# Kernel optimization log

Hardware: AMD Instinct MI355X
Metric: run time of the kernel (lower is better)

The kernel has to match this reference:

```python
import jax, jax.numpy as jnp
import numpy as np

B, H, W, C = 16, 64, 64, 512
NH, WS, SS, P = 16, 8, 4, 4
HID = 2048
N = WS * WS
HD = C // NH
SCALE = HD ** -0.5
NWIN = (H // WS) * (W // WS)

# static azimuth angle table (N, N): (w_i - w_j) * 2*pi / W_res  (W_res = input_resolution[1])
_wf = np.arange(N) % WS
AZ_ANG = (_wf[:, None] - _wf[None, :]).astype(np.float32) * np.float32(2.0 * np.pi / W)


def _shift_mask():
    # standard SW-MSA region mask: 0 within same region, -100 across regions
    img = np.zeros((H, W), dtype=np.float32)
    cnt = 0
    for hs in (slice(0, -WS), slice(-WS, -SS), slice(-SS, None)):
        for ws_ in (slice(0, -WS), slice(-WS, -SS), slice(-SS, None)):
            img[hs, ws_] = cnt
            cnt += 1
    win = img.reshape(H // WS, WS, W // WS, WS).transpose(0, 2, 1, 3).reshape(-1, N)
    diff = win[:, None, :] - win[:, :, None]
    return np.where(diff != 0, -100.0, 0.0).astype(np.float32)

MASK = _shift_mask()  # (NWIN, N, N)


def _ln(x, g, b):
    m = x.mean(-1, keepdims=True)
    v = ((x - m) ** 2).mean(-1, keepdims=True)
    return (x - m) / jnp.sqrt(v + 1e-5) * g + b


def _forward(x, D, gamma1, beta1, Wqkv, bqkv, Wproj, bproj, a_p, b_p, a_r, b_r, gamma2, beta2, W1, b1, W2, b2):
    shortcut = x
    h = _ln(x, gamma1, beta1).reshape(B, H, W, C)
    d = D.reshape(B, H, W)
    # cyclic shift
    h = jnp.roll(h, (-SS, -SS), axis=(1, 2))
    d = jnp.roll(d, (-SS, -SS), axis=(1, 2))
    # window partition -> (B*NWIN, N, C) and depth windows (B*NWIN, N)
    hw = h.reshape(B, H // WS, WS, W // WS, WS, C).transpose(0, 1, 3, 2, 4, 5).reshape(-1, N, C)
    dw = d.reshape(B, H // WS, WS, W // WS, WS).transpose(0, 1, 3, 2, 4).reshape(-1, N)
    Bw = B * NWIN
    qkv = (hw @ Wqkv + bqkv).reshape(Bw, N, 3, NH, HD)
    q, k, v = qkv[:, :, 0], qkv[:, :, 1], qkv[:, :, 2]
    attn = jnp.einsum('bnhd,bmhd->bhnm', q * SCALE, k)
    # Fourier azimuth bias A_phi: (NH, N, N), input-independent within forward
    i_arr = jnp.arange(1, P + 1, dtype=x.dtype)
    az_i = i_arr[:, None, None] * jnp.asarray(AZ_ANG, dtype=x.dtype)  # (P, N, N)
    A_phi = (jnp.einsum('pnm,ph->hnm', jnp.cos(az_i), a_p[1:])
             + jnp.einsum('pnm,ph->hnm', jnp.sin(az_i), b_p)) / P + a_p[0][:, None, None]
    # Fourier radial bias A_r from input-dependent depth differences; r_max hardcoded to 2 in source
    radD = dw[:, None, :] - dw[:, :, None]  # (Bw, N, N): D_j - D_i
    ang = radD[None] * (np.pi * i_arr)[:, None, None, None]  # (P, Bw, N, N); 2*pi*i/r_max = pi*i
    A_r = (jnp.einsum('pbnm,ph->bhnm', jnp.cos(ang), a_r[1:])
           + jnp.einsum('pbnm,ph->bhnm', jnp.sin(ang), b_r)) / P + a_r[0][None, :, None, None]
    attn = attn + A_phi[None] + A_r
    attn = attn.reshape(B, NWIN, NH, N, N) + jnp.asarray(MASK, dtype=x.dtype)[None, :, None]
    attn = jax.nn.softmax(attn.reshape(Bw, NH, N, N), axis=-1)
    out = jnp.einsum('bhnm,bmhd->bnhd', attn, v).reshape(Bw, N, C)
    out = out @ Wproj + bproj
    # window reverse + reverse shift
    out = out.reshape(B, H // WS, W // WS, WS, WS, C).transpose(0, 1, 3, 2, 4, 5).reshape(B, H, W, C)
    out = jnp.roll(out, (SS, SS), axis=(1, 2)).reshape(B, H * W, C)
    x2 = shortcut + out
    h2 = _ln(x2, gamma2, beta2)
    h2 = jax.nn.gelu(h2 @ W1 + b1, approximate=False) @ W2 + b2
    return x2 + h2


def setup_inputs() -> dict:
    key = jax.random.key(0)
    ks = jax.random.split(key, 10)
    s = 0.02
    return {
        'x': jax.random.normal(ks[0], (B, H * W, C), jnp.float32),
        'D': jax.random.uniform(ks[1], (B, H * W), jnp.float32),
        'gamma1': jnp.ones((C,), jnp.float32),
        'beta1': jnp.zeros((C,), jnp.float32),
        'Wqkv': jax.random.normal(ks[2], (C, 3 * C), jnp.float32) * s,
        'bqkv': jnp.zeros((3 * C,), jnp.float32),
        'Wproj': jax.random.normal(ks[3], (C, C), jnp.float32) * s,
        'bproj': jnp.zeros((C,), jnp.float32),
        'a_p': jax.random.normal(ks[4], (P + 1, NH), jnp.float32) * s,
        'b_p': jax.random.normal(ks[5], (P, NH), jnp.float32) * s,
        'a_r': jax.random.normal(ks[6], (P + 1, NH), jnp.float32) * s,
        'b_r': jax.random.normal(ks[7], (P, NH), jnp.float32) * s,
        'gamma2': jnp.ones((C,), jnp.float32),
        'beta2': jnp.zeros((C,), jnp.float32),
        'W1': jax.random.normal(ks[8], (C, HID), jnp.float32) * s,
        'b1': jnp.zeros((HID,), jnp.float32),
        'W2': jax.random.normal(ks[9], (HID, C), jnp.float32) * s,
        'b2': jnp.zeros((C,), jnp.float32),
    }


def reference(x, D, gamma1, beta1, Wqkv, bqkv, Wproj, bproj, a_p, b_p, a_r, b_r, gamma2, beta2, W1, b1, W2, b2):
    return _forward(x, D, gamma1, beta1, Wqkv, bqkv, Wproj, bproj, a_p, b_p, a_r, b_r, gamma2, beta2, W1, b1, W2, b2)
```

## Files before the change

kernel.cpp:

```cpp
#include <hip/hip_runtime.h>
#include <hip/hip_bf16.h>
#include <cstdint>


typedef __attribute__((ext_vector_type(8))) short short8;
typedef __attribute__((ext_vector_type(4))) float f32x4;
typedef unsigned short u16;

__device__ __forceinline__ u16 f2bf(float f) {
  __hip_bfloat16 h = __float2bfloat16(f);
  return *reinterpret_cast<u16*>(&h);
}

__device__ __forceinline__ void gld_lds16(const u16* g, u16* l) {
  __builtin_amdgcn_global_load_lds(
      (const __attribute__((address_space(1))) void*)g,
      (__attribute__((address_space(3))) void*)l, 16, 0, 0);
}

__global__ void wt_convert(const float* __restrict__ W, u16* __restrict__ Wt,
                           int K, int N) {
  __shared__ float tile[32][33];
  const int n0 = blockIdx.x * 32, k0 = blockIdx.y * 32;
  const int tx = threadIdx.x & 31, ty = threadIdx.x >> 5;
#pragma unroll
  for (int r = ty; r < 32; r += 8)
    tile[r][tx] = W[(size_t)(k0 + r) * N + n0 + tx];
  __syncthreads();
#pragma unroll
  for (int r = ty; r < 32; r += 8)
    Wt[(size_t)(n0 + r) * K + k0 + tx] = f2bf(tile[tx][r]);
}

__global__ void aphi_kernel(const float* __restrict__ a_p,
                            const float* __restrict__ b_p,
                            float* __restrict__ aphi) {
  const int idx = blockIdx.x * 256 + threadIdx.x;
  const int h = idx >> 12, n = (idx >> 6) & 63, m = idx & 63;
  const float ang = (float)((n & 7) - (m & 7)) * 0.09817477042468103f;
  float v = a_p[h];
#pragma unroll
  for (int p = 0; p < 4; ++p) {
    float s, c;
    __sincosf((float)(p + 1) * ang, &s, &c);
    v += (c * a_p[(p + 1) * 16 + h] + s * b_p[p * 16 + h]) * 0.25f;
  }
  aphi[idx] = v;
}

__global__ __launch_bounds__(64) void ln1_win(
    const float* __restrict__ x, const float* __restrict__ D,
    const float* __restrict__ gamma, const float* __restrict__ beta,
    u16* __restrict__ xw, float* __restrict__ dwout) {
  const int r = blockIdx.x;
  const int lane = threadIdx.x;
  const int w = r >> 6, n = r & 63;
  const int bb = w >> 6, nw = w & 63;
  const int wh = nw >> 3, ww = nw & 7;
  const int i = n >> 3, j = n & 7;
  const int sh = (wh * 8 + i + 4) & 63;
  const int sw = (ww * 8 + j + 4) & 63;
  const size_t src = ((size_t)bb * 4096 + sh * 64 + sw) * 512;
  float4 v0 = *(const float4*)(x + src + lane * 8);
  float4 v1 = *(const float4*)(x + src + lane * 8 + 4);
  float vv[8] = {v0.x, v0.y, v0.z, v0.w, v1.x, v1.y, v1.z, v1.w};
  float s = 0.f, s2 = 0.f;
#pragma unroll
  for (int e = 0; e < 8; ++e) { s += vv[e]; s2 += vv[e] * vv[e]; }
#pragma unroll
  for (int off = 32; off > 0; off >>= 1) {
    s += __shfl_xor(s, off);
    s2 += __shfl_xor(s2, off);
  }
  const float mean = s * (1.0f / 512.0f);
  const float var = s2 * (1.0f / 512.0f) - mean * mean;
  const float rstd = rsqrtf(var + 1e-5f);
  const int c0 = lane * 8;
  u16 ob[8];
#pragma unroll
  for (int e = 0; e < 8; ++e)
    ob[e] = f2bf((vv[e] - mean) * rstd * gamma[c0 + e] + beta[c0 + e]);
  *(short8*)(xw + (size_t)r * 512 + c0) = *(short8*)ob;
  if (lane == 0) dwout[r] = D[(size_t)bb * 4096 + sh * 64 + sw];
}

__global__ __launch_bounds__(64) void ln2_kernel(
    const float* __restrict__ xin, const float* __restrict__ gamma,
    const float* __restrict__ beta, u16* __restrict__ h2) {
  const int r = blockIdx.x;
  const int lane = threadIdx.x;
  const size_t src = (size_t)r * 512;
  float4 v0 = *(const float4*)(xin + src + lane * 8);
  float4 v1 = *(const float4*)(xin + src + lane * 8 + 4);
  float vv[8] = {v0.x, v0.y, v0.z, v0.w, v1.x, v1.y, v1.z, v1.w};
  float s = 0.f, s2 = 0.f;
#pragma unroll
  for (int e = 0; e < 8; ++e) { s += vv[e]; s2 += vv[e] * vv[e]; }
#pragma unroll
  for (int off = 32; off > 0; off >>= 1) {
    s += __shfl_xor(s, off);
    s2 += __shfl_xor(s2, off);
  }
  const float mean = s * (1.0f / 512.0f);
  const float var = s2 * (1.0f / 512.0f) - mean * mean;
  const float rstd = rsqrtf(var + 1e-5f);
  const int c0 = lane * 8;
  u16 ob[8];
#pragma unroll
  for (int e = 0; e < 8; ++e)
    ob[e] = f2bf((vv[e] - mean) * rstd * gamma[c0 + e] + beta[c0 + e]);
  *(short8*)(h2 + src + c0) = *(short8*)ob;
}

template <int EPI, int GX>
__global__ __launch_bounds__(512, 4) void gemm_bt(
    const u16* __restrict__ A, const u16* __restrict__ Bt,
    const float* __restrict__ bias, u16* __restrict__ outb,
    float* __restrict__ outf, const float* __restrict__ addsrc,
    int M, int N, int K) {
  __shared__ __align__(16) u16 sA[256 * 32];
  __shared__ __align__(16) u16 sB[128 * 32];
  const int t = threadIdx.x;
  const int lid = blockIdx.x;
  const int xcd = lid & 7;
  const int tt = lid >> 3;
  const int bx = tt % GX;
  const int by = (tt / GX) * 8 + xcd;
  const int m0 = by * 256, n0 = bx * 128;
  const int lane = t & 63, wave = t >> 6;
  const int wm = wave >> 1, wn = wave & 1;
  const int l15 = lane & 15, quad = lane >> 4;

  f32x4 acc[4][4];
#pragma unroll
  for (int i = 0; i < 4; ++i)
#pragma unroll
    for (int j = 0; j < 4; ++j) acc[i][j] = (f32x4){0.f, 0.f, 0.f, 0.f};

  const int sa0 = t, sa1 = t + 512, sb0 = t;
  const int ra0 = sa0 >> 2, pa0 = sa0 & 3, la0 = pa0 ^ ((ra0 >> 1) & 3);
  const int ra1 = sa1 >> 2, pa1 = sa1 & 3, la1 = pa1 ^ ((ra1 >> 1) & 3);
  const int rb0 = sb0 >> 2, pb0 = sb0 & 3, lb0c = pb0 ^ ((rb0 >> 1) & 3);
  const u16* Ag0 = A + (size_t)(m0 + ra0) * K + la0 * 8;
  const u16* Ag1 = A + (size_t)(m0 + ra1) * K + la1 * 8;
  const u16* Bg0 = Bt + (size_t)(n0 + rb0) * K + lb0c * 8;
  u16* lA0 = &sA[sa0 * 8];
  u16* lA1 = &sA[sa1 * 8];
  u16* lB0 = &sB[sb0 * 8];

  for (int kk = 0; kk < K; kk += 32) {
    gld_lds16(Ag0 + kk, lA0);
    gld_lds16(Ag1 + kk, lA1);
    gld_lds16(Bg0 + kk, lB0);
    __syncthreads();
    short8 af[4], bf[4];
#pragma unroll
    for (int i = 0; i < 4; ++i) {
      const int ra = wm * 64 + i * 16 + l15;
      const int ca = quad ^ ((ra >> 1) & 3);
      af[i] = *(const short8*)&sA[ra * 32 + ca * 8];
      const int rb = wn * 64 + i * 16 + l15;
      const int cb = quad ^ ((rb >> 1) & 3);
      bf[i] = *(const short8*)&sB[rb * 32 + cb * 8];
    }
#pragma unroll
    for (int i = 0; i < 4; ++i)
#pragma unroll
      for (int j = 0; j < 4; ++j)
        acc[i][j] = __builtin_amdgcn_mfma_f32_16x16x32_bf16(af[i], bf[j],
                                                            acc[i][j], 0, 0, 0);
    __syncthreads();
  }

#pragma unroll
  for (int i = 0; i < 4; ++i) {
    const int gr0 = m0 + wm * 64 + i * 16 + quad * 4;
#pragma unroll
    for (int j = 0; j < 4; ++j) {
      const int gc = n0 + wn * 64 + j * 16 + l15;
      const float bv = bias[gc];
      f32x4 a = acc[i][j];
#pragma unroll
      for (int r = 0; r < 4; ++r) {
        const int gr = gr0 + r;
        float val = a[r] + bv;
        if (EPI == 0) {
          outb[(size_t)gr * N + gc] = f2bf(val);
        } else if (EPI == 1) {
          val = 0.5f * val * (1.0f + erff(val * 0.7071067811865475f));
          outb[(size_t)gr * N + gc] = f2bf(val);
        } else if (EPI == 2) {
          const int w = gr >> 6, n = gr & 63;
          const int bb = w >> 6, nw = w & 63;
          const int wh = nw >> 3, ww = nw & 7;
          const int ii = n >> 3, jj = n & 7;
          const int th = (wh * 8 + ii + 4) & 63;
          const int tw = (ww * 8 + jj + 4) & 63;
          const size_t tok = (size_t)bb * 4096 + th * 64 + tw;
          outf[tok * 512 + gc] = addsrc[tok * 512 + gc] + val;
        } else {
          outf[(size_t)gr * N + gc] += val;
        }
      }
    }
  }
}

__device__ __forceinline__ int bandf(int p) {
  return p < 56 ? 0 : (p < 60 ? 1 : 2);
}

__global__ void attn_kernel(const u16* __restrict__ qkv,
                            const float* __restrict__ dw,
                            const float* __restrict__ aphi,
                            const float* __restrict__ a_r,
                            const float* __restrict__ b_r,
                            u16* __restrict__ outp) {
  __shared__ __align__(16) u16 sVt[32 * 72];
  __shared__ __align__(16) u16 sP[64 * 72];
  __shared__ float sdw[64];
  const int bid = blockIdx.x;
  const int w = bid >> 4, h = bid & 15;
  const int lane = threadIdx.x;
  const int l15 = lane & 15, quad = lane >> 4;
  const int nw = w & 63, wh = nw >> 3, wwc = nw & 7;

  const float ar0 = a_r[h];
  float arc[4], brc[4];
#pragma unroll
  for (int p = 0; p < 4; ++p) {
    arc[p] = a_r[(p + 1) * 16 + h] * 0.25f;
    brc[p] = b_r[p * 16 + h] * 0.25f;
  }

  sdw[lane] = dw[w * 64 + lane];
  {
    const u16* vrow = qkv + (size_t)(w * 64 + lane) * 1536 + 1024 + h * 32;
    u16 vt[32];
#pragma unroll
    for (int c = 0; c < 4; ++c)
      *(short8*)&vt[c * 8] = *(const short8*)(vrow + c * 8);
#pragma unroll
    for (int d = 0; d < 32; ++d) sVt[d * 72 + lane] = vt[d];
  }
  __syncthreads();

  short8 qf[4], kf[4];
#pragma unroll
  for (int tq = 0; tq < 4; ++tq) {
    qf[tq] = *(const short8*)(qkv + (size_t)(w * 64 + tq * 16 + l15) * 1536 +
                              h * 32 + quad * 8);
    kf[tq] = *(const short8*)(qkv + (size_t)(w * 64 + tq * 16 + l15) * 1536 +
                              512 + h * 32 + quad * 8);
  }

  float dn[16];
  int rq[16];
#pragma unroll
  for (int tm = 0; tm < 4; ++tm)
#pragma unroll
    for (int r = 0; r < 4; ++r) {
      const int n = tm * 16 + quad * 4 + r;
      dn[tm * 4 + r] = sdw[n];
      rq[tm * 4 + r] = bandf(wh * 8 + (n >> 3)) * 4 + bandf(wwc * 8 + (n & 7));
    }
  float dmv[4];
  int rk[4];
#pragma unroll
  for (int tn = 0; tn < 4; ++tn) {
    const int m = tn * 16 + l15;
    dmv[tn] = sdw[m];
    rk[tn] = bandf(wh * 8 + (m >> 3)) * 4 + bandf(wwc * 8 + (m & 7));
  }

  f32x4 S[4][4];
  const float SCALE = 0.17677669529663687f;
#pragma unroll
  for (int tm = 0; tm < 4; ++tm)
#pragma unroll
    for (int tn = 0; tn < 4; ++tn) {
      f32x4 s = __builtin_amdgcn_mfma_f32_16x16x32_bf16(
          qf[tm], kf[tn], (f32x4){0.f, 0.f, 0.f, 0.f}, 0, 0, 0);
      const int m = tn * 16 + l15;
#pragma unroll
      for (int r = 0; r < 4; ++r) {
        const int n = tm * 16 + quad * 4 + r;
        const float rad = dmv[tn] - dn[tm * 4 + r];
        float s1, c1;
        __sincosf(3.14159265358979323846f * rad, &s1, &c1);
        const float c2 = c1 * c1 - s1 * s1, t2 = 2.f * s1 * c1;
        const float c3 = c2 * c1 - t2 * s1, t3 = t2 * c1 + c2 * s1;
        const float c4 = c2 * c2 - t2 * t2, t4 = 2.f * t2 * c2;
        const float arv = ar0 + c1 * arc[0] + s1 * brc[0] + c2 * arc[1] +
                          t2 * brc[1] + c3 * arc[2] + t3 * brc[2] +
                          c4 * arc[3] + t4 * brc[3];
        float val = s[r] * SCALE + aphi[h * 4096 + n * 64 + m] + arv;
        if (rq[tm * 4 + r] != rk[tn]) val -= 100.f;
        S[tm][tn][r] = val;
      }
    }

#pragma unroll
  for (int tm = 0; tm < 4; ++tm)
#pragma unroll
    for (int r = 0; r < 4; ++r) {
      float mx = fmaxf(fmaxf(S[tm][0][r], S[tm][1][r]),
                       fmaxf(S[tm][2][r], S[tm][3][r]));
#pragma unroll
      for (int off = 1; off < 16; off <<= 1) mx = fmaxf(mx, __shfl_xor(mx, off));
      float sm = 0.f;
#pragma unroll
      for (int tn = 0; tn < 4; ++tn) {
        const float e = __expf(S[tm][tn][r] - mx);
        S[tm][tn][r] = e;
        sm += e;
      }
#pragma unroll
      for (int off = 1; off < 16; off <<= 1) sm += __shfl_xor(sm, off);
      const float inv = 1.0f / sm;
      const int n = tm * 16 + quad * 4 + r;
#pragma unroll
      for (int tn = 0; tn < 4; ++tn)
        sP[n * 72 + tn * 16 + l15] = f2bf(S[tm][tn][r] * inv);
    }
  __syncthreads();

  short8 vf[2][2];
#pragma unroll
  for (int ks = 0; ks < 2; ++ks)
#pragma unroll
    for (int td = 0; td < 2; ++td)
      vf[ks][td] =
          *(const short8*)&sVt[(td * 16 + l15) * 72 + ks * 32 + quad * 8];
  f32x4 O[4][2];
#pragma unroll
  for (int tm = 0; tm < 4; ++tm)
#pragma unroll
    for (int td = 0; td < 2; ++td) O[tm][td] = (f32x4){0.f, 0.f, 0.f, 0.f};
#pragma unroll
  for (int tm = 0; tm < 4; ++tm)
#pragma unroll
    for (int ks = 0; ks < 2; ++ks) {
      const short8 pf =
          *(const short8*)&sP[(tm * 16 + l15) * 72 + ks * 32 + quad * 8];
#pragma unroll
      for (int td = 0; td < 2; ++td)
        O[tm][td] =
            __builtin_amdgcn_mfma_f32_16x16x32_bf16(pf, vf[ks][td], O[tm][td], 0, 0, 0);
    }

#pragma unroll
  for (int tm = 0; tm < 4; ++tm)
#pragma unroll
    for (int td = 0; td < 2; ++td)
#pragma unroll
      for (int r = 0; r < 4; ++r) {
        const int n = tm * 16 + quad * 4 + r;
        const int d = td * 16 + l15;
        outp[(size_t)(w * 64 + n) * 512 + h * 32 + d] = f2bf(O[tm][td][r]);
      }
}

extern "C" void kernel_launch(void* const* d_in, const int* in_sizes, int n_in,
                              void* d_out, int out_size, void* d_ws,
                              size_t ws_size, hipStream_t stream) {
  const float* x = (const float*)d_in[0];
  const float* D = (const float*)d_in[1];
  const float* gamma1 = (const float*)d_in[2];
  const float* beta1 = (const float*)d_in[3];
  const float* Wqkv = (const float*)d_in[4];
  const float* bqkv = (const float*)d_in[5];
  const float* Wproj = (const float*)d_in[6];
  const float* bproj = (const float*)d_in[7];
  const float* a_p = (const float*)d_in[8];
  const float* b_p = (const float*)d_in[9];
  const float* a_r = (const float*)d_in[10];
  const float* b_r = (const float*)d_in[11];
  const float* gamma2 = (const float*)d_in[12];
  const float* beta2 = (const float*)d_in[13];
  const float* W1 = (const float*)d_in[14];
  const float* b1 = (const float*)d_in[15];
  const float* W2 = (const float*)d_in[16];
  const float* b2 = (const float*)d_in[17];
  float* out = (float*)d_out;

  char* ws = (char*)d_ws;
  const size_t OFF_XW = 0;
  const size_t OFF_QKV = 67108864;
  const size_t OFF_AO = 335544320;
  const size_t OFF_WQT = 402653184;
  const size_t OFF_WPT = 404226048;
  const size_t OFF_W1T = 404750336;
  const size_t OFF_W2T = 406847488;
  const size_t OFF_APHI = 408944640;
  const size_t OFF_DW = 409206784;
  const size_t TOTAL = 409468928;
  if (ws_size < TOTAL) return;

  u16* xw = (u16*)(ws + OFF_XW);
  u16* qkv = (u16*)(ws + OFF_QKV);
  u16* ao = (u16*)(ws + OFF_AO);
  u16* WqkvT = (u16*)(ws + OFF_WQT);
  u16* WprojT = (u16*)(ws + OFF_WPT);
  u16* W1T = (u16*)(ws + OFF_W1T);
  u16* W2T = (u16*)(ws + OFF_W2T);
  float* aphiW = (float*)(ws + OFF_APHI);
  float* dwW = (float*)(ws + OFF_DW);
  u16* h2 = xw;
  u16* gbuf = qkv;

  wt_convert<<<dim3(48, 16), 256, 0, stream>>>(Wqkv, WqkvT, 512, 1536);
  wt_convert<<<dim3(16, 16), 256, 0, stream>>>(Wproj, WprojT, 512, 512);
  wt_convert<<<dim3(64, 16), 256, 0, stream>>>(W1, W1T, 512, 2048);
  wt_convert<<<dim3(16, 64), 256, 0, stream>>>(W2, W2T, 2048, 512);
  aphi_kernel<<<256, 256, 0, stream>>>(a_p, b_p, aphiW);
  ln1_win<<<65536, 64, 0, stream>>>(x, D, gamma1, beta1, xw, dwW);

  gemm_bt<0, 12><<<12 * 256, 512, 0, stream>>>(xw, WqkvT, bqkv, qkv, nullptr,
                                               nullptr, 65536, 1536, 512);
  attn_kernel<<<16384, 64, 0, stream>>>(qkv, dwW, aphiW, a_r, b_r, ao);
  gemm_bt<2, 4><<<4 * 256, 512, 0, stream>>>(ao, WprojT, bproj, nullptr, out,
                                             x, 65536, 512, 512);
  ln2_kernel<<<65536, 64, 0, stream>>>(out, gamma2, beta2, h2);
  gemm_bt<1, 16><<<16 * 256, 512, 0, stream>>>(h2, W1T, b1, gbuf, nullptr,
                                               nullptr, 65536, 2048, 512);
  gemm_bt<3, 4><<<4 * 256, 512, 0, stream>>>(gbuf, W2T, b2, nullptr, out,
                                             nullptr, 65536, 512, 2048);
}
```

Baseline: 1.097 ms.

## Triple-buffer GEMM LDS tiles with async global-to-LDS prefetch

The bf16 GEMM kernel now keeps three LDS stages for the A and B tiles and prefetches two k-tiles ahead using direct global-to-LDS loads. Hand-written vmcnt waits and barriers replace the per-iteration syncthreads, so global load latency can overlap with MFMA work. The cost is three times the LDS footprint, 72KB per block, which can limit occupancy below the launch_bounds target of 4 blocks. It also depends on vmcnt counting that is fragile if the compiler inserts other vector memory ops.

```diff
diff --git a/kernel.cpp b/kernel.cpp
--- a/kernel.cpp
+++ b/kernel.cpp
@@ -118,8 +118,8 @@
     const float* __restrict__ bias, u16* __restrict__ outb,
     float* __restrict__ outf, const float* __restrict__ addsrc,
     int M, int N, int K) {
-  __shared__ __align__(16) u16 sA[256 * 32];
-  __shared__ __align__(16) u16 sB[128 * 32];
+  __shared__ __align__(16) u16 sA[3][256 * 32];
+  __shared__ __align__(16) u16 sB[3][128 * 32];
   const int t = threadIdx.x;
   const int lid = blockIdx.x;
   const int xcd = lid & 7;
@@ -144,32 +144,51 @@
   const u16* Ag0 = A + (size_t)(m0 + ra0) * K + la0 * 8;
   const u16* Ag1 = A + (size_t)(m0 + ra1) * K + la1 * 8;
   const u16* Bg0 = Bt + (size_t)(n0 + rb0) * K + lb0c * 8;
-  u16* lA0 = &sA[sa0 * 8];
-  u16* lA1 = &sA[sa1 * 8];
-  u16* lB0 = &sB[sb0 * 8];
-
-  for (int kk = 0; kk < K; kk += 32) {
-    gld_lds16(Ag0 + kk, lA0);
-    gld_lds16(Ag1 + kk, lA1);
-    gld_lds16(Bg0 + kk, lB0);
-    __syncthreads();
-    short8 af[4], bf[4];
+
+  const int NT = K >> 5;
+
+#pragma unroll
+  for (int pt = 0; pt < 3; ++pt) {
+    gld_lds16(Ag0 + pt * 32, &sA[pt][sa0 * 8]);
+    gld_lds16(Ag1 + pt * 32, &sA[pt][sa1 * 8]);
+    gld_lds16(Bg0 + pt * 32, &sB[pt][sb0 * 8]);
+  }
+
+  int buf = 0;
+  for (int kt = 0; kt < NT; ++kt) {
+    if (kt + 2 < NT) {
+      asm volatile("s_waitcnt vmcnt(6)\n\ts_barrier" ::: "memory");
+    } else if (kt + 1 < NT) {
+      asm volatile("s_waitcnt vmcnt(3)\n\ts_barrier" ::: "memory");
+    } else {
+      asm volatile("s_waitcnt vmcnt(0)\n\ts_barrier" ::: "memory");
+    }
+    const u16* bufA = sA[buf];
+    const u16* bufB = sB[buf];
+    short8 af[4], bfr[4];
 #pragma unroll
     for (int i = 0; i < 4; ++i) {
       const int ra = wm * 64 + i * 16 + l15;
       const int ca = quad ^ ((ra >> 1) & 3);
-      af[i] = *(const short8*)&sA[ra * 32 + ca * 8];
+      af[i] = *(const short8*)&bufA[ra * 32 + ca * 8];
       const int rb = wn * 64 + i * 16 + l15;
       const int cb = quad ^ ((rb >> 1) & 3);
-      bf[i] = *(const short8*)&sB[rb * 32 + cb * 8];
+      bfr[i] = *(const short8*)&bufB[rb * 32 + cb * 8];
     }
 #pragma unroll
     for (int i = 0; i < 4; ++i)
 #pragma unroll
       for (int j = 0; j < 4; ++j)
-        acc[i][j] = __builtin_amdgcn_mfma_f32_16x16x32_bf16(af[i], bf[j],
+        acc[i][j] = __builtin_amdgcn_mfma_f32_16x16x32_bf16(af[i], bfr[j],
                                                             acc[i][j], 0, 0, 0);
-    __syncthreads();
+    asm volatile("s_waitcnt lgkmcnt(0)\n\ts_barrier" ::: "memory");
+    if (kt + 3 < NT) {
+      const int kk = (kt + 3) * 32;
+      gld_lds16(Ag0 + kk, &sA[buf][sa0 * 8]);
+      gld_lds16(Ag1 + kk, &sA[buf][sa1 * 8]);
+      gld_lds16(Bg0 + kk, &sB[buf][sb0 * 8]);
+    }
+    buf = (buf == 2) ? 0 : buf + 1;
   }
 
 #pragma unroll
```

Result: faster. 1.075 ms (-2.0%).

## Rewrite GEMM as double-buffered 256x256 tile pipeline with interleaved prefetch

Applied to the files above, without the earlier changes.

Replaces the single-buffered 256x128 GEMM mainloop with a 256x256 tile and a 64-wide K step. LDS is double-buffered and split into two K-halves, and the next tile's A and B loads are issued between MFMA phases under explicit vmcnt waits, barriers and s_setprio. The aim is to hide global-to-LDS latency and raise MFMA work per LDS byte. In exchange it uses 128KB of LDS and 128 accumulator registers per thread, so occupancy drops to about one block per CU. Grid sizes are halved to match the wider N tile.

```diff
diff --git a/kernel.cpp b/kernel.cpp
--- a/kernel.cpp
+++ b/kernel.cpp
@@ -112,69 +112,152 @@
   *(short8*)(h2 + src + c0) = *(short8*)ob;
 }
 
+#define MFMA_BF16 __builtin_amdgcn_mfma_f32_16x16x32_bf16
+#define SBAR __builtin_amdgcn_s_barrier()
+#define SCHED0 __builtin_amdgcn_sched_barrier(0)
+#define WAIT_LGKM0 asm volatile("s_waitcnt lgkmcnt(0)" ::: "memory")
+
 template <int EPI, int GX>
-__global__ __launch_bounds__(512, 4) void gemm_bt(
+__global__ __launch_bounds__(512, 2) void gemm_bt(
     const u16* __restrict__ A, const u16* __restrict__ Bt,
     const float* __restrict__ bias, u16* __restrict__ outb,
     float* __restrict__ outf, const float* __restrict__ addsrc,
     int M, int N, int K) {
-  __shared__ __align__(16) u16 sA[256 * 32];
-  __shared__ __align__(16) u16 sB[128 * 32];
+  __shared__ __align__(16) u16 sA[2][16384];
+  __shared__ __align__(16) u16 sB[2][16384];
   const int t = threadIdx.x;
   const int lid = blockIdx.x;
   const int xcd = lid & 7;
   const int tt = lid >> 3;
   const int bx = tt % GX;
   const int by = (tt / GX) * 8 + xcd;
-  const int m0 = by * 256, n0 = bx * 128;
+  const int m0 = by * 256, n0 = bx * 256;
   const int lane = t & 63, wave = t >> 6;
-  const int wm = wave >> 1, wn = wave & 1;
+  const int wm = wave >> 2, wn = wave & 3;
   const int l15 = lane & 15, quad = lane >> 4;
 
-  f32x4 acc[4][4];
-#pragma unroll
-  for (int i = 0; i < 4; ++i)
+  f32x4 acc[8][4];
+#pragma unroll
+  for (int i = 0; i < 8; ++i)
 #pragma unroll
     for (int j = 0; j < 4; ++j) acc[i][j] = (f32x4){0.f, 0.f, 0.f, 0.f};
 
-  const int sa0 = t, sa1 = t + 512, sb0 = t;
-  const int ra0 = sa0 >> 2, pa0 = sa0 & 3, la0 = pa0 ^ ((ra0 >> 1) & 3);
-  const int ra1 = sa1 >> 2, pa1 = sa1 & 3, la1 = pa1 ^ ((ra1 >> 1) & 3);
-  const int rb0 = sb0 >> 2, pb0 = sb0 & 3, lb0c = pb0 ^ ((rb0 >> 1) & 3);
-  const u16* Ag0 = A + (size_t)(m0 + ra0) * K + la0 * 8;
-  const u16* Ag1 = A + (size_t)(m0 + ra1) * K + la1 * 8;
-  const u16* Bg0 = Bt + (size_t)(n0 + rb0) * K + lb0c * 8;
-  u16* lA0 = &sA[sa0 * 8];
-  u16* lA1 = &sA[sa1 * 8];
-  u16* lB0 = &sB[sb0 * 8];
-
-  for (int kk = 0; kk < K; kk += 32) {
-    gld_lds16(Ag0 + kk, lA0);
-    gld_lds16(Ag1 + kk, lA1);
-    gld_lds16(Bg0 + kk, lB0);
-    __syncthreads();
-    short8 af[4], bf[4];
-#pragma unroll
-    for (int i = 0; i < 4; ++i) {
-      const int ra = wm * 64 + i * 16 + l15;
-      const int ca = quad ^ ((ra >> 1) & 3);
-      af[i] = *(const short8*)&sA[ra * 32 + ca * 8];
-      const int rb = wn * 64 + i * 16 + l15;
-      const int cb = quad ^ ((rb >> 1) & 3);
-      bf[i] = *(const short8*)&sB[rb * 32 + cb * 8];
-    }
-#pragma unroll
-    for (int i = 0; i < 4; ++i)
-#pragma unroll
-      for (int j = 0; j < 4; ++j)
-        acc[i][j] = __builtin_amdgcn_mfma_f32_16x16x32_bf16(af[i], bf[j],
-                                                            acc[i][j], 0, 0, 0);
-    __syncthreads();
-  }
-
-#pragma unroll
-  for (int i = 0; i < 4; ++i) {
-    const int gr0 = m0 + wm * 64 + i * 16 + quad * 4;
+  const int sr0 = t >> 2, sp0 = t & 3;
+  const int sr1 = (t + 512) >> 2, sp1 = (t + 512) & 3;
+  const int sc0 = sp0 ^ ((sr0 >> 1) & 3);
+  const int sc1 = sp1 ^ ((sr1 >> 1) & 3);
+  const int od0 = t * 8, od1 = (t + 512) * 8;
+  const u16* AgL0 = A + (size_t)(m0 + sr0) * K + sc0 * 8;
+  const u16* AgL1 = A + (size_t)(m0 + sr1) * K + sc1 * 8;
+  const u16* BgL0 = Bt + (size_t)(n0 + sr0) * K + sc0 * 8;
+  const u16* BgL1 = Bt + (size_t)(n0 + sr1) * K + sc1 * 8;
+
+#define STAGE_A(nb_, kh_, kt_)                                        \
+  do {                                                                \
+    gld_lds16(AgL0 + (kt_) * 64 + (kh_) * 32,                         \
+              &sA[nb_][(kh_) * 8192 + od0]);                          \
+    gld_lds16(AgL1 + (kt_) * 64 + (kh_) * 32,                         \
+              &sA[nb_][(kh_) * 8192 + od1]);                          \
+  } while (0)
+#define STAGE_B(nb_, kh_, kt_)                                        \
+  do {                                                                \
+    gld_lds16(BgL0 + (kt_) * 64 + (kh_) * 32,                         \
+              &sB[nb_][(kh_) * 8192 + od0]);                          \
+    gld_lds16(BgL1 + (kt_) * 64 + (kh_) * 32,                         \
+              &sB[nb_][(kh_) * 8192 + od1]);                          \
+  } while (0)
+
+  const int NT = K >> 6;
+
+  const int pch8 = (quad ^ ((l15 >> 1) & 3)) * 8;
+  const int aro = (wm * 128 + l15) * 32 + pch8;
+  const int bro = (wn * 64 + l15) * 32 + pch8;
+
+  STAGE_A(0, 0, 0);
+  STAGE_B(0, 0, 0);
+  STAGE_A(0, 1, 0);
+  STAGE_B(0, 1, 0);
+
+  for (int kt = 0; kt < NT; ++kt) {
+    const int b = kt & 1, nb = b ^ 1;
+    const bool pf = (kt + 1 < NT);
+    short8 a0[8], bb0, bb1;
+    if (pf) {
+      STAGE_A(nb, 0, kt + 1);
+      asm volatile("s_waitcnt vmcnt(6)" ::: "memory");
+    } else {
+      asm volatile("s_waitcnt vmcnt(4)" ::: "memory");
+    }
+    SBAR;
+#pragma unroll
+    for (int i = 0; i < 8; ++i) a0[i] = *(const short8*)&sA[b][aro + i * 512];
+    bb0 = *(const short8*)&sB[b][bro];
+    bb1 = *(const short8*)&sB[b][bro + 512];
+    WAIT_LGKM0;
+    SCHED0;
+    __builtin_amdgcn_s_setprio(1);
+#pragma unroll
+    for (int i = 0; i < 8; ++i) acc[i][0] = MFMA_BF16(a0[i], bb0, acc[i][0], 0, 0, 0);
+#pragma unroll
+    for (int i = 0; i < 8; ++i) acc[i][1] = MFMA_BF16(a0[i], bb1, acc[i][1], 0, 0, 0);
+    __builtin_amdgcn_s_setprio(0);
+    SCHED0;
+    SBAR;
+    if (pf) STAGE_B(nb, 0, kt + 1);
+    bb0 = *(const short8*)&sB[b][bro + 1024];
+    bb1 = *(const short8*)&sB[b][bro + 1536];
+    SBAR;
+    WAIT_LGKM0;
+    SCHED0;
+    __builtin_amdgcn_s_setprio(1);
+#pragma unroll
+    for (int i = 0; i < 8; ++i) acc[i][2] = MFMA_BF16(a0[i], bb0, acc[i][2], 0, 0, 0);
+#pragma unroll
+    for (int i = 0; i < 8; ++i) acc[i][3] = MFMA_BF16(a0[i], bb1, acc[i][3], 0, 0, 0);
+    __builtin_amdgcn_s_setprio(0);
+    SCHED0;
+    SBAR;
+    if (pf) {
+      STAGE_A(nb, 1, kt + 1);
+      asm volatile("s_waitcnt vmcnt(6)" ::: "memory");
+    } else {
+      asm volatile("s_waitcnt vmcnt(0)" ::: "memory");
+    }
+    SBAR;
+#pragma unroll
+    for (int i = 0; i < 8; ++i)
+      a0[i] = *(const short8*)&sA[b][8192 + aro + i * 512];
+    bb0 = *(const short8*)&sB[b][8192 + bro];
+    bb1 = *(const short8*)&sB[b][8192 + bro + 512];
+    WAIT_LGKM0;
+    SCHED0;
+    __builtin_amdgcn_s_setprio(1);
+#pragma unroll
+    for (int i = 0; i < 8; ++i) acc[i][0] = MFMA_BF16(a0[i], bb0, acc[i][0], 0, 0, 0);
+#pragma unroll
+    for (int i = 0; i < 8; ++i) acc[i][1] = MFMA_BF16(a0[i], bb1, acc[i][1], 0, 0, 0);
+    __builtin_amdgcn_s_setprio(0);
+    SCHED0;
+    SBAR;
+    if (pf) STAGE_B(nb, 1, kt + 1);
+    bb0 = *(const short8*)&sB[b][8192 + bro + 1024];
+    bb1 = *(const short8*)&sB[b][8192 + bro + 1536];
+    SBAR;
+    WAIT_LGKM0;
+    SCHED0;
+    __builtin_amdgcn_s_setprio(1);
+#pragma unroll
+    for (int i = 0; i < 8; ++i) acc[i][2] = MFMA_BF16(a0[i], bb0, acc[i][2], 0, 0, 0);
+#pragma unroll
+    for (int i = 0; i < 8; ++i) acc[i][3] = MFMA_BF16(a0[i], bb1, acc[i][3], 0, 0, 0);
+    __builtin_amdgcn_s_setprio(0);
+    SCHED0;
+    SBAR;
+  }
+
+#pragma unroll
+  for (int i = 0; i < 8; ++i) {
+    const int gr0 = m0 + wm * 128 + i * 16 + quad * 4;
 #pragma unroll
     for (int j = 0; j < 4; ++j) {
       const int gc = n0 + wn * 64 + j * 16 + l15;
@@ -416,14 +499,14 @@
   aphi_kernel<<<256, 256, 0, stream>>>(a_p, b_p, aphiW);
   ln1_win<<<65536, 64, 0, stream>>>(x, D, gamma1, beta1, xw, dwW);
 
-  gemm_bt<0, 12><<<12 * 256, 512, 0, stream>>>(xw, WqkvT, bqkv, qkv, nullptr,
-                                               nullptr, 65536, 1536, 512);
+  gemm_bt<0, 6><<<6 * 256, 512, 0, stream>>>(xw, WqkvT, bqkv, qkv, nullptr,
+                                             nullptr, 65536, 1536, 512);
   attn_kernel<<<16384, 64, 0, stream>>>(qkv, dwW, aphiW, a_r, b_r, ao);
-  gemm_bt<2, 4><<<4 * 256, 512, 0, stream>>>(ao, WprojT, bproj, nullptr, out,
+  gemm_bt<2, 2><<<2 * 256, 512, 0, stream>>>(ao, WprojT, bproj, nullptr, out,
                                              x, 65536, 512, 512);
   ln2_kernel<<<65536, 64, 0, stream>>>(out, gamma2, beta2, h2);
-  gemm_bt<1, 16><<<16 * 256, 512, 0, stream>>>(h2, W1T, b1, gbuf, nullptr,
-                                               nullptr, 65536, 2048, 512);
-  gemm_bt<3, 4><<<4 * 256, 512, 0, stream>>>(gbuf, W2T, b2, nullptr, out,
+  gemm_bt<1, 8><<<8 * 256, 512, 0, stream>>>(h2, W1T, b1, gbuf, nullptr,
+                                             nullptr, 65536, 2048, 512);
+  gemm_bt<3, 2><<<2 * 256, 512, 0, stream>>>(gbuf, W2T, b2, nullptr, out,
                                              nullptr, 65536, 512, 2048);
 }
```

Result: slower. 1.299 ms (+18.5%).

## Enlarge GEMM tile to 256x256 with register-prefetched double-buffered LDS

Applied to the files above, without the earlier changes.

Rewrites the bf16 GEMM to use 256x256 output tiles with a K-step of 64, 8x4 MFMA tiles per wave, and double-buffered LDS filled from register-staged global loads issued one iteration ahead. Direct global-to-LDS loads are replaced by ordinary loads plus LDS stores, which removes one barrier per iteration and overlaps the next tile's loads with compute. Grid sizes are halved to match. The larger tile raises data reuse but also raises register and LDS pressure, and occupancy bounds drop to 2 blocks per CU.

```diff
diff --git a/kernel.cpp b/kernel.cpp
--- a/kernel.cpp
+++ b/kernel.cpp
@@ -10,12 +10,6 @@
 __device__ __forceinline__ u16 f2bf(float f) {
   __hip_bfloat16 h = __float2bfloat16(f);
   return *reinterpret_cast<u16*>(&h);
-}
-
-__device__ __forceinline__ void gld_lds16(const u16* g, u16* l) {
-  __builtin_amdgcn_global_load_lds(
-      (const __attribute__((address_space(1))) void*)g,
-      (__attribute__((address_space(3))) void*)l, 16, 0, 0);
 }
 
 __global__ void wt_convert(const float* __restrict__ W, u16* __restrict__ Wt,
@@ -112,69 +106,109 @@
   *(short8*)(h2 + src + c0) = *(short8*)ob;
 }
 
+#define MFMA_BF16 __builtin_amdgcn_mfma_f32_16x16x32_bf16
+
 template <int EPI, int GX>
-__global__ __launch_bounds__(512, 4) void gemm_bt(
+__global__ __launch_bounds__(512, 2) void gemm_bt(
     const u16* __restrict__ A, const u16* __restrict__ Bt,
     const float* __restrict__ bias, u16* __restrict__ outb,
     float* __restrict__ outf, const float* __restrict__ addsrc,
     int M, int N, int K) {
-  __shared__ __align__(16) u16 sA[256 * 32];
-  __shared__ __align__(16) u16 sB[128 * 32];
+  __shared__ __align__(16) u16 sA[32768];
+  __shared__ __align__(16) u16 sB[32768];
   const int t = threadIdx.x;
   const int lid = blockIdx.x;
   const int xcd = lid & 7;
   const int tt = lid >> 3;
   const int bx = tt % GX;
   const int by = (tt / GX) * 8 + xcd;
-  const int m0 = by * 256, n0 = bx * 128;
+  const int m0 = by * 256, n0 = bx * 256;
   const int lane = t & 63, wave = t >> 6;
-  const int wm = wave >> 1, wn = wave & 1;
+  const int wm = wave >> 2, wn = wave & 3;
   const int l15 = lane & 15, quad = lane >> 4;
 
-  f32x4 acc[4][4];
-#pragma unroll
-  for (int i = 0; i < 4; ++i)
+  f32x4 acc[8][4];
+#pragma unroll
+  for (int i = 0; i < 8; ++i)
 #pragma unroll
     for (int j = 0; j < 4; ++j) acc[i][j] = (f32x4){0.f, 0.f, 0.f, 0.f};
 
-  const int sa0 = t, sa1 = t + 512, sb0 = t;
-  const int ra0 = sa0 >> 2, pa0 = sa0 & 3, la0 = pa0 ^ ((ra0 >> 1) & 3);
-  const int ra1 = sa1 >> 2, pa1 = sa1 & 3, la1 = pa1 ^ ((ra1 >> 1) & 3);
-  const int rb0 = sb0 >> 2, pb0 = sb0 & 3, lb0c = pb0 ^ ((rb0 >> 1) & 3);
-  const u16* Ag0 = A + (size_t)(m0 + ra0) * K + la0 * 8;
-  const u16* Ag1 = A + (size_t)(m0 + ra1) * K + la1 * 8;
-  const u16* Bg0 = Bt + (size_t)(n0 + rb0) * K + lb0c * 8;
-  u16* lA0 = &sA[sa0 * 8];
-  u16* lA1 = &sA[sa1 * 8];
-  u16* lB0 = &sB[sb0 * 8];
-
-  for (int kk = 0; kk < K; kk += 32) {
-    gld_lds16(Ag0 + kk, lA0);
-    gld_lds16(Ag1 + kk, lA1);
-    gld_lds16(Bg0 + kk, lB0);
+  const int r0 = t >> 2, c0 = t & 3;
+  const int wo0 = r0 * 32 + ((c0 ^ ((r0 >> 1) & 3)) * 8);
+  const int wo1 = (r0 + 128) * 32 + ((c0 ^ (((r0 + 128) >> 1) & 3)) * 8);
+  const u16* Ag0 = A + (size_t)(m0 + r0) * K + c0 * 8;
+  const u16* Ag1 = A + (size_t)(m0 + r0 + 128) * K + c0 * 8;
+  const u16* Bg0 = Bt + (size_t)(n0 + r0) * K + c0 * 8;
+  const u16* Bg1 = Bt + (size_t)(n0 + r0 + 128) * K + c0 * 8;
+
+  const int NT = K >> 6;
+
+  const int pch8 = (quad ^ ((l15 >> 1) & 3)) * 8;
+  const int aro = (wm * 128 + l15) * 32 + pch8;
+  const int bro = (wn * 64 + l15) * 32 + pch8;
+
+  short8 rA0 = *(const short8*)(Ag0);
+  short8 rA1 = *(const short8*)(Ag1);
+  short8 rA2 = *(const short8*)(Ag0 + 32);
+  short8 rA3 = *(const short8*)(Ag1 + 32);
+  short8 rB0 = *(const short8*)(Bg0);
+  short8 rB1 = *(const short8*)(Bg1);
+  short8 rB2 = *(const short8*)(Bg0 + 32);
+  short8 rB3 = *(const short8*)(Bg1 + 32);
+
+  for (int kt = 0; kt < NT; ++kt) {
+    const int bo = (kt & 1) << 14;
+    *(short8*)&sA[bo + wo0] = rA0;
+    *(short8*)&sA[bo + wo1] = rA1;
+    *(short8*)&sA[bo + 8192 + wo0] = rA2;
+    *(short8*)&sA[bo + 8192 + wo1] = rA3;
+    *(short8*)&sB[bo + wo0] = rB0;
+    *(short8*)&sB[bo + wo1] = rB1;
+    *(short8*)&sB[bo + 8192 + wo0] = rB2;
+    *(short8*)&sB[bo + 8192 + wo1] = rB3;
     __syncthreads();
-    short8 af[4], bf[4];
-#pragma unroll
-    for (int i = 0; i < 4; ++i) {
-      const int ra = wm * 64 + i * 16 + l15;
-      const int ca = quad ^ ((ra >> 1) & 3);
-      af[i] = *(const short8*)&sA[ra * 32 + ca * 8];
-      const int rb = wn * 64 + i * 16 + l15;
-      const int cb = quad ^ ((rb >> 1) & 3);
-      bf[i] = *(const short8*)&sB[rb * 32 + cb * 8];
-    }
-#pragma unroll
-    for (int i = 0; i < 4; ++i)
-#pragma unroll
-      for (int j = 0; j < 4; ++j)
-        acc[i][j] = __builtin_amdgcn_mfma_f32_16x16x32_bf16(af[i], bf[j],
-                                                            acc[i][j], 0, 0, 0);
-    __syncthreads();
-  }
-
-#pragma unroll
-  for (int i = 0; i < 4; ++i) {
-    const int gr0 = m0 + wm * 64 + i * 16 + quad * 4;
+    if (kt + 1 < NT) {
+      const int ko = (kt + 1) * 64;
+      rA0 = *(const short8*)(Ag0 + ko);
+      rA1 = *(const short8*)(Ag1 + ko);
+      rA2 = *(const short8*)(Ag0 + ko + 32);
+      rA3 = *(const short8*)(Ag1 + ko + 32);
+      rB0 = *(const short8*)(Bg0 + ko);
+      rB1 = *(const short8*)(Bg1 + ko);
+      rB2 = *(const short8*)(Bg0 + ko + 32);
+      rB3 = *(const short8*)(Bg1 + ko + 32);
+    }
+    const u16* bA = &sA[bo];
+    const u16* bB = &sB[bo];
+#pragma unroll
+    for (int kh = 0; kh < 2; ++kh) {
+      const int kho = kh * 8192;
+      short8 a0[8];
+#pragma unroll
+      for (int i = 0; i < 8; ++i)
+        a0[i] = *(const short8*)&bA[kho + aro + i * 512];
+      const short8 b0 = *(const short8*)&bB[kho + bro];
+      const short8 b1 = *(const short8*)&bB[kho + bro + 512];
+      const short8 b2 = *(const short8*)&bB[kho + bro + 1024];
+      const short8 b3 = *(const short8*)&bB[kho + bro + 1536];
+#pragma unroll
+      for (int i = 0; i < 8; ++i)
+        acc[i][0] = MFMA_BF16(a0[i], b0, acc[i][0], 0, 0, 0);
+#pragma unroll
+      for (int i = 0; i < 8; ++i)
+        acc[i][1] = MFMA_BF16(a0[i], b1, acc[i][1], 0, 0, 0);
+#pragma unroll
+      for (int i = 0; i < 8; ++i)
+        acc[i][2] = MFMA_BF16(a0[i], b2, acc[i][2], 0, 0, 0);
+#pragma unroll
+      for (int i = 0; i < 8; ++i)
+        acc[i][3] = MFMA_BF16(a0[i], b3, acc[i][3], 0, 0, 0);
+    }
+  }
+
+#pragma unroll
+  for (int i = 0; i < 8; ++i) {
+    const int gr0 = m0 + wm * 128 + i * 16 + quad * 4;
 #pragma unroll
     for (int j = 0; j < 4; ++j) {
       const int gc = n0 + wn * 64 + j * 16 + l15;
@@ -416,14 +450,14 @@
   aphi_kernel<<<256, 256, 0, stream>>>(a_p, b_p, aphiW);
   ln1_win<<<65536, 64, 0, stream>>>(x, D, gamma1, beta1, xw, dwW);
 
-  gemm_bt<0, 12><<<12 * 256, 512, 0, stream>>>(xw, WqkvT, bqkv, qkv, nullptr,
-                                               nullptr, 65536, 1536, 512);
+  gemm_bt<0, 6><<<6 * 256, 512, 0, stream>>>(xw, WqkvT, bqkv, qkv, nullptr,
+                                             nullptr, 65536, 1536, 512);
   attn_kernel<<<16384, 64, 0, stream>>>(qkv, dwW, aphiW, a_r, b_r, ao);
-  gemm_bt<2, 4><<<4 * 256, 512, 0, stream>>>(ao, WprojT, bproj, nullptr, out,
+  gemm_bt<2, 2><<<2 * 256, 512, 0, stream>>>(ao, WprojT, bproj, nullptr, out,
                                              x, 65536, 512, 512);
   ln2_kernel<<<65536, 64, 0, stream>>>(out, gamma2, beta2, h2);
-  gemm_bt<1, 16><<<16 * 256, 512, 0, stream>>>(h2, W1T, b1, gbuf, nullptr,
-                                               nullptr, 65536, 2048, 512);
-  gemm_bt<3, 4><<<4 * 256, 512, 0, stream>>>(gbuf, W2T, b2, nullptr, out,
+  gemm_bt<1, 8><<<8 * 256, 512, 0, stream>>>(h2, W1T, b1, gbuf, nullptr,
+                                             nullptr, 65536, 2048, 512);
+  gemm_bt<3, 2><<<2 * 256, 512, 0, stream>>>(gbuf, W2T, b2, nullptr, out,
                                              nullptr, 65536, 512, 2048);
 }
```

Result: no change. 1.085 ms (-1.1%).
